# Optimization experiments

Hardware: AMD Instinct MI355X
Metric: run time of the kernel (lower is better)

The kernel has to match this reference:

```python
import jax, jax.numpy as jnp
import numpy as np

B, DIM, H, W = 2, 256, 64, 64
HEADS, DIM_HEAD = 8, 64
DIM_INNER = HEADS * DIM_HEAD  # 512


def setup_inputs() -> dict:
    key = jax.random.key(0)
    k1, k2, k3 = jax.random.split(key, 3)
    fmap = jax.random.normal(k1, (B, DIM, H, W), dtype=jnp.float32)
    # 1x1 convs == channel matmuls; store as [out_ch, in_ch]
    w_qkv = jax.random.normal(k2, (3 * DIM_INNER, DIM), dtype=jnp.float32) * (DIM ** -0.5)
    w_out = jax.random.normal(k3, (DIM, DIM_INNER), dtype=jnp.float32) * (DIM_INNER ** -0.5)
    return {"fmap": fmap, "w_qkv": w_qkv, "w_out": w_out}


def reference(fmap, w_qkv, w_out):
    b, c, x, y = fmap.shape
    n = x * y
    h, d = HEADS, DIM_HEAD
    xt = fmap.reshape(b, c, n)                       # [B, C, N]
    qkv = jnp.einsum('oc,bcn->bon', w_qkv, xt)        # [B, 3*h*d, N]
    q, k, v = jnp.split(qkv, 3, axis=1)               # each [B, h*d, N]
    # -> [B, h, N, d]
    to_bhnd = lambda t: t.reshape(b, h, d, n).transpose(0, 1, 3, 2)
    q, k, v = to_bhnd(q), to_bhnd(k), to_bhnd(v)
    # Euclidean distance matrix (torch.cdist p=2)
    q2 = jnp.sum(q * q, axis=-1)                      # [B, h, N]
    k2 = jnp.sum(k * k, axis=-1)                      # [B, h, N]
    qk = jnp.einsum('bhid,bhjd->bhij', q, k)          # [B, h, N, N]
    sim = jnp.sqrt(jnp.maximum(q2[..., :, None] + k2[..., None, :] - 2.0 * qk, 0.0))
    attn = jax.nn.softmax(sim, axis=-1)
    out = jnp.einsum('bhij,bhjd->bhid', attn, v)      # [B, h, N, d]
    out = out.transpose(0, 1, 3, 2).reshape(b, h * d, n)  # [B, h*d, N]
    out = jnp.einsum('oc,bcn->bon', w_out, out)       # [B, dim, N]
    return out.reshape(b, c, x, y)
```

## Files before the change

### kernel.cpp

```cpp
#include <hip/hip_runtime.h>

#define B_      2
#define DIM_    256
#define N_      4096
#define HEADS_  8
#define DINNER_ 512

typedef _Float16 half_t;
typedef _Float16 half8  __attribute__((ext_vector_type(8)));
typedef _Float16 half4v __attribute__((ext_vector_type(4)));
typedef _Float16 half2v __attribute__((ext_vector_type(2)));
typedef float    floatx4 __attribute__((ext_vector_type(4)));

#define SCL_    1.4426950408889634f
#define SHIFT2_ 20.0f


__global__ __launch_bounds__(256) void prep_all(const float* __restrict__ fmap,
                                                const float* __restrict__ w_qkv,
                                                const float* __restrict__ w_out,
                                                half_t* __restrict__ wqF,
                                                half_t* __restrict__ woF,
                                                half_t* __restrict__ xTg) {
    const int t = threadIdx.x, bx = blockIdx.x;
    __shared__ float Tl[64 * 68];
    if (bx < 96) {
        half_t* dst = wqF + (size_t)bx * 4096;
#pragma unroll
        for (int j = 0; j < 2; ++j) {
            const int cch = j * 256 + t;
            const int o = cch >> 4, m15 = cch & 15;
            const float4 a  = *(const float4*)&w_qkv[(size_t)(bx * 16 + m15) * 256 + o * 8];
            const float4 bb = *(const float4*)&w_qkv[(size_t)(bx * 16 + m15) * 256 + o * 8 + 4];
            half8 hv;
            hv[0] = (half_t)a.x;  hv[1] = (half_t)a.y;  hv[2] = (half_t)a.z;  hv[3] = (half_t)a.w;
            hv[4] = (half_t)bb.x; hv[5] = (half_t)bb.y; hv[6] = (half_t)bb.z; hv[7] = (half_t)bb.w;
            *(half8*)(dst + o * 128 + m15 * 8) = hv;
        }
    } else if (bx < 112) {
        const int mt = bx - 96;
        half_t* dst = woF + (size_t)mt * 8192;
#pragma unroll
        for (int j = 0; j < 4; ++j) {
            const int cch = j * 256 + t;
            const int o = cch >> 4, m15 = cch & 15;
            const float4 a  = *(const float4*)&w_out[(size_t)(mt * 16 + m15) * 512 + o * 8];
            const float4 bb = *(const float4*)&w_out[(size_t)(mt * 16 + m15) * 512 + o * 8 + 4];
            half8 hv;
            hv[0] = (half_t)a.x;  hv[1] = (half_t)a.y;  hv[2] = (half_t)a.z;  hv[3] = (half_t)a.w;
            hv[4] = (half_t)bb.x; hv[5] = (half_t)bb.y; hv[6] = (half_t)bb.z; hv[7] = (half_t)bb.w;
            *(half8*)(dst + o * 128 + m15 * 8) = hv;
        }
    } else {
        const int idx = bx - 112;
        const int n0 = (idx & 63) * 64, k0 = ((idx >> 6) & 3) * 64, b = idx >> 8;
        {
            const int kk = t >> 2, nq = (t & 3) * 16;
#pragma unroll
            for (int q = 0; q < 4; ++q) {
                float4 v = *(const float4*)&fmap[((size_t)b * DIM_ + k0 + kk) * N_ + n0 + nq + 4 * q];
                *(float4*)&Tl[kk * 68 + nq + 4 * q] = v;
            }
        }
        __syncthreads();
        {
            const int n = t >> 2, ko = (t & 3) * 16;
            half8 h0, h1;
#pragma unroll
            for (int j = 0; j < 8; ++j) h0[j] = (half_t)Tl[(ko + j) * 68 + n];
#pragma unroll
            for (int j = 0; j < 8; ++j) h1[j] = (half_t)Tl[(ko + 8 + j) * 68 + n];
            half_t* dst = xTg + (((size_t)b * 64 + (n0 >> 6)) * 4 + (k0 >> 6)) * 4096;
            const int o0 = ((ko >> 5) * 4 + (n >> 4)) * 512 + (((ko >> 3) & 3) * 16 + (n & 15)) * 8;
            const int k8 = ko + 8;
            const int o1 = ((k8 >> 5) * 4 + (n >> 4)) * 512 + (((k8 >> 3) & 3) * 16 + (n & 15)) * 8;
            *(half8*)(dst + o0) = h0;
            *(half8*)(dst + o1) = h1;
        }
    }
}

__global__ __launch_bounds__(256) void mm_qkv_mf(const half_t* __restrict__ wqF,
                                                 const half_t* __restrict__ xTg,
                                                 half_t* __restrict__ perm,
                                                 float* __restrict__ sq) {
    const int nt64 = blockIdx.x, by = blockIdx.y, b = blockIdx.z;
    const int t = threadIdx.x, w = t >> 6, L = t & 63, c = L & 15, g = L >> 4;
    const int mt = by * 4 + w;

    const half_t* Ab = wqF + (size_t)mt * 4096;
    const half_t* Bb = xTg + (((size_t)b * 64 + nt64) * 4) * 4096;

    __shared__ __align__(16) char smraw[16384];
    half_t* Bsh = (half_t*)smraw;
    half_t* VtH = (half_t*)smraw;
    float*  red = (float*)(smraw + 8192);

    const floatx4 fz = {0.f, 0.f, 0.f, 0.f};
    floatx4 acc[4];
#pragma unroll
    for (int ns = 0; ns < 4; ++ns) acc[ns] = fz;

#pragma unroll
    for (int ph = 0; ph < 2; ++ph) {
        if (ph) __syncthreads();
#pragma unroll
        for (int j = 0; j < 4; ++j)
            *(half8*)&Bsh[(j * 256 + t) * 8] = *(const half8*)(Bb + ph * 8192 + (j * 256 + t) * 8);
        __syncthreads();
#pragma unroll
        for (int kk = 0; kk < 4; ++kk) {
            const int kc = ph * 4 + kk;
            const half8 af = *(const half8*)(Ab + (kc * 4 + g) * 128 + c * 8);
            const half_t* Bs = Bsh + (kk >> 1) * 4096 + (kk & 1) * 2048;
#pragma unroll
            for (int ns = 0; ns < 4; ++ns) {
                const half8 bf = *(const half8*)(Bs + ns * 512 + L * 8);
                acc[ns] = __builtin_amdgcn_mfma_f32_16x16x32_f16(af, bf, acc[ns], 0, 0, 0);
            }
        }
    }
    __syncthreads();

    half_t* dst = perm + (((size_t)(b * 24 + by) * 64 + nt64) << 12);
    if (by < 16) {
        const float qs = (by < 8) ? -2.0f : 1.0f;
        float part[4];
#pragma unroll
        for (int ns = 0; ns < 4; ++ns) {
            half_t m[4];
            float s = 0.f;
#pragma unroll
            for (int i = 0; i < 4; ++i) {
                const half_t hq = (half_t)(acc[ns][i] * SCL_);
                const float f = (float)hq;
                s = fmaf(f, f, s);
                m[i] = (half_t)(qs * f);
            }
            part[ns] = s;
            const int off = ((w >> 1) * 4 + ns) * 512 + (((2 * w + (g >> 1)) & 3) * 16 + c) * 8 + 4 * (g & 1);
            half2v p0v, p1v;
            p0v[0] = m[0]; p0v[1] = m[1];
            p1v[0] = m[2]; p1v[1] = m[3];
            *(half2v*)(VtH + off)     = p0v;
            *(half2v*)(VtH + off + 2) = p1v;
        }
#pragma unroll
        for (int ns = 0; ns < 4; ++ns)
            red[(ns * 16 + (w * 4 + g)) * 17 + c] = part[ns];
        __syncthreads();
#pragma unroll
        for (int j = 0; j < 2; ++j)
            *(half8*)(dst + t * 16 + j * 8) = *(half8*)(VtH + t * 16 + j * 8);
        if (t < 64) {
            const int ns = t >> 4, cc = t & 15;
            float s = 0.f;
#pragma unroll
            for (int wg = 0; wg < 16; ++wg) s += red[(ns * 16 + wg) * 17 + cc];
            const int tens = by >> 3, hh = by & 7;
            sq[((size_t)(tens * 16 + b * 8 + hh)) * N_ + nt64 * 64 + ns * 16 + cc] = s;
        }
    } else {
#pragma unroll
        for (int ns = 0; ns < 4; ++ns)
#pragma unroll
            for (int i = 0; i < 4; ++i)
                VtH[((ns >> 1) * 4 + w) * 512 + ((c >> 2) * 16 + 4 * g + i) * 8 + (ns & 1) * 4 + (c & 3)] =
                    (half_t)acc[ns][i];
        __syncthreads();
#pragma unroll
        for (int j = 0; j < 2; ++j)
            *(half8*)(dst + t * 16 + j * 8) = *(half8*)(VtH + t * 16 + j * 8);
    }
}

__global__ __launch_bounds__(512) void attn_mfma(const half_t* __restrict__ perm,
                                                 const float* __restrict__ sq,
                                                 half_t* __restrict__ oh,
                                                 float* __restrict__ lbuf) {
    const int bx = blockIdx.x;
    const int qb = bx & 15, kh = bx >> 4;
    const int h = blockIdx.y, b = blockIdx.z;
    const int bh = b * HEADS_ + h;

    const half_t* Qb = perm + ((size_t)(b * 24 + h) << 18);
    const half_t* Kb = perm + ((size_t)(b * 24 + 8 + h) << 18);
    const half_t* Vb = perm + ((size_t)(b * 24 + 16 + h) << 18);
    const float* q2a = sq + (size_t)bh * N_;
    const float* k2a = sq + (size_t)(16 + bh) * N_;

    __shared__ __align__(16) half_t Kl[2][4096];
    __shared__ __align__(16) half_t Vl[2][4096];
    __shared__ __align__(16) unsigned int k2lp[1024];

    const int t = threadIdx.x, w = t >> 6, L = t & 63, c = L & 15, g = L >> 4;
    const floatx4 fz = {0.f, 0.f, 0.f, 0.f};

    {
        const float2 kv = *(const float2*)&k2a[kh * 1024 + t * 2];
        const half_t h0 = (half_t)kv.x; const half_t l0 = (half_t)(kv.x - (float)h0);
        const half_t h1 = (half_t)kv.y; const half_t l1 = (half_t)(kv.y - (float)h1);
        k2lp[t * 2]     = (unsigned)__builtin_bit_cast(unsigned short, h0) |
                          ((unsigned)__builtin_bit_cast(unsigned short, l0) << 16);
        k2lp[t * 2 + 1] = (unsigned)__builtin_bit_cast(unsigned short, h1) |
                          ((unsigned)__builtin_bit_cast(unsigned short, l1) << 16);
    }

    const int tl = w >> 1;
    const int p0 = (w & 1) * 2, p1 = p0 + 1;
    const half_t* Qt = Qb + ((size_t)(qb * 4 + tl) << 12);
    const half8 bq0a = *(const half8*)(Qt + (0 * 4 + p0) * 512 + L * 8);
    const half8 bq1a = *(const half8*)(Qt + (1 * 4 + p0) * 512 + L * 8);
    const half8 bq0b = *(const half8*)(Qt + (0 * 4 + p1) * 512 + L * 8);
    const half8 bq1b = *(const half8*)(Qt + (1 * 4 + p1) * 512 + L * 8);

    union U8 { half8 v; unsigned int u[4]; };
    U8 qXa, qXb;
    {
        const float q2la = q2a[qb * 256 + 64 * tl + 16 * p0 + c];
        const float q2lb = q2a[qb * 256 + 64 * tl + 16 * p1 + c];
        const half_t ha = (half_t)q2la; const half_t la = (half_t)(q2la - (float)ha);
        const half_t hb = (half_t)q2lb; const half_t lb_ = (half_t)(q2lb - (float)hb);
        const unsigned pka = (unsigned)__builtin_bit_cast(unsigned short, ha) |
                             ((unsigned)__builtin_bit_cast(unsigned short, la) << 16);
        const unsigned pkb = (unsigned)__builtin_bit_cast(unsigned short, hb) |
                             ((unsigned)__builtin_bit_cast(unsigned short, lb_) << 16);
        const bool lo16 = (L < 16);
        qXa.u[0] = lo16 ? pka : 0u; qXa.u[1] = lo16 ? 0x3C003C00u : 0u;
        qXa.u[2] = 0u; qXa.u[3] = 0u;
        qXb.u[0] = lo16 ? pkb : 0u; qXb.u[1] = lo16 ? 0x3C003C00u : 0u;
        qXb.u[2] = 0u; qXb.u[3] = 0u;
    }

    half8 aone8;
    {
        const half_t ov = (c == 0) ? (half_t)1.0f : (half_t)0.0f;
        aone8[0] = ov; aone8[1] = ov; aone8[2] = ov; aone8[3] = ov;
        aone8[4] = ov; aone8[5] = ov; aone8[6] = ov; aone8[7] = ov;
    }

    floatx4 Oa[4], Ob[4];
    floatx4 laca = fz, lacb = fz;
#pragma unroll
    for (int dt = 0; dt < 4; ++dt) { Oa[dt] = fz; Ob[dt] = fz; }

    const int kt0 = kh * 16;
    half8 rk = *(const half8*)(Kb + ((size_t)kt0 << 12) + t * 8);
    half8 rv = *(const half8*)(Vb + ((size_t)kt0 << 12) + t * 8);

    union H8 { half8 v; half2v h2[4]; };

#define QKC(J, SA, SB) { \
    const half8 ak0 = *(const half8*)(&Kl[buf][(0 * 4 + (J)) * 512 + L * 8]); \
    const half8 ak1 = *(const half8*)(&Kl[buf][(1 * 4 + (J)) * 512 + L * 8]); \
    U8 kX; kX.u[0] = 0x3C003C00u; kX.u[1] = k2lp[it * 64 + (J) * 16 + c]; \
    kX.u[2] = 0u; kX.u[3] = 0u; \
    SA = __builtin_amdgcn_mfma_f32_16x16x32_f16(ak0, bq0a, fz, 0, 0, 0); \
    SA = __builtin_amdgcn_mfma_f32_16x16x32_f16(ak1, bq1a, SA, 0, 0, 0); \
    SA = __builtin_amdgcn_mfma_f32_16x16x32_f16(kX.v, qXa.v, SA, 0, 0, 0); \
    SB = __builtin_amdgcn_mfma_f32_16x16x32_f16(ak0, bq0b, fz, 0, 0, 0); \
    SB = __builtin_amdgcn_mfma_f32_16x16x32_f16(ak1, bq1b, SB, 0, 0, 0); \
    SB = __builtin_amdgcn_mfma_f32_16x16x32_f16(kX.v, qXb.v, SB, 0, 0, 0); }

#define SMX(SA, SB, SLOT, UA, UB) { \
    float pa[4], pb[4]; \
    _Pragma("unroll") \
    for (int i = 0; i < 4; ++i) { \
        pa[i] = __builtin_amdgcn_exp2f(__builtin_amdgcn_sqrtf(__builtin_fabsf(SA[i])) - SHIFT2_); \
        pb[i] = __builtin_amdgcn_exp2f(__builtin_amdgcn_sqrtf(__builtin_fabsf(SB[i])) - SHIFT2_); } \
    UA.h2[2 * (SLOT)]     = __builtin_bit_cast(half2v, __builtin_amdgcn_cvt_pkrtz(pa[0], pa[1])); \
    UA.h2[2 * (SLOT) + 1] = __builtin_bit_cast(half2v, __builtin_amdgcn_cvt_pkrtz(pa[2], pa[3])); \
    UB.h2[2 * (SLOT)]     = __builtin_bit_cast(half2v, __builtin_amdgcn_cvt_pkrtz(pb[0], pb[1])); \
    UB.h2[2 * (SLOT) + 1] = __builtin_bit_cast(half2v, __builtin_amdgcn_cvt_pkrtz(pb[2], pb[3])); }

#define LPV(NTP, UA, UB) { \
    laca = __builtin_amdgcn_mfma_f32_16x16x32_f16(aone8, UA.v, laca, 0, 0, 0); \
    lacb = __builtin_amdgcn_mfma_f32_16x16x32_f16(aone8, UB.v, lacb, 0, 0, 0); \
    _Pragma("unroll") \
    for (int dt = 0; dt < 4; ++dt) { \
        const half8 av = *(const half8*)(&Vl[buf][((NTP) * 4 + dt) * 512 + L * 8]); \
        Oa[dt] = __builtin_amdgcn_mfma_f32_16x16x32_f16(av, UA.v, Oa[dt], 0, 0, 0); \
        Ob[dt] = __builtin_amdgcn_mfma_f32_16x16x32_f16(av, UB.v, Ob[dt], 0, 0, 0); } }

    for (int it = 0; it < 16; ++it) {
        const int buf = it & 1;
        *(half8*)(&Kl[buf][t * 8]) = rk;
        *(half8*)(&Vl[buf][t * 8]) = rv;
        asm volatile("s_waitcnt lgkmcnt(0)\n\ts_barrier" ::: "memory");
        if (it < 15) {
            rk = *(const half8*)(Kb + ((size_t)(kt0 + it + 1) << 12) + t * 8);
            rv = *(const half8*)(Vb + ((size_t)(kt0 + it + 1) << 12) + t * 8);
        }

        floatx4 S0a, S0b, S1a, S1b, S2a, S2b, S3a, S3b;
        H8 u0a, u0b, u1a, u1b;
        QKC(0, S0a, S0b)
        QKC(1, S1a, S1b)
        SMX(S0a, S0b, 0, u0a, u0b)
        QKC(2, S2a, S2b)
        SMX(S1a, S1b, 1, u0a, u0b)
        QKC(3, S3a, S3b)
        SMX(S2a, S2b, 0, u1a, u1b)
        LPV(0, u0a, u0b)
        SMX(S3a, S3b, 1, u1a, u1b)
        LPV(1, u1a, u1b)
    }
#undef QKC
#undef SMX
#undef LPV

    const int ntile = qb * 4 + tl;
    half_t* dst = oh + (size_t)kh * 4194304 + (((size_t)bh * 64 + ntile) << 12);
#pragma unroll
    for (int dt = 0; dt < 4; ++dt) {
        const int obase = ((dt >> 1) * 4) * 512 + (((2 * dt + (g >> 1)) & 3) * 16 + c) * 8 + 4 * (g & 1);
        const half2v a0 = __builtin_bit_cast(half2v, __builtin_amdgcn_cvt_pkrtz(Oa[dt][0], Oa[dt][1]));
        const half2v a1 = __builtin_bit_cast(half2v, __builtin_amdgcn_cvt_pkrtz(Oa[dt][2], Oa[dt][3]));
        *(half2v*)(dst + obase + p0 * 512)     = a0;
        *(half2v*)(dst + obase + p0 * 512 + 2) = a1;
        const half2v b0 = __builtin_bit_cast(half2v, __builtin_amdgcn_cvt_pkrtz(Ob[dt][0], Ob[dt][1]));
        const half2v b1 = __builtin_bit_cast(half2v, __builtin_amdgcn_cvt_pkrtz(Ob[dt][2], Ob[dt][3]));
        *(half2v*)(dst + obase + p1 * 512)     = b0;
        *(half2v*)(dst + obase + p1 * 512 + 2) = b1;
    }
    if (L < 16) {
        const size_t lb0 = (size_t)kh * 65536 + (size_t)bh * N_ + qb * 256 + 64 * tl;
        lbuf[lb0 + 16 * p0 + L] = laca[0];
        lbuf[lb0 + 16 * p1 + L] = lacb[0];
    }
}

__global__ __launch_bounds__(256) void mm_out_mf(const half_t* __restrict__ woF,
                                                 const half_t* __restrict__ oh,
                                                 const float* __restrict__ lbuf,
                                                 float* __restrict__ out) {
    const int nt64 = blockIdx.x, mb = blockIdx.y, b = blockIdx.z;
    const int t = threadIdx.x, w = t >> 6, L = t & 63, c = L & 15, g = L >> 4;
    const int mt = mb * 4 + w;

    const half_t* Ab = woF + (size_t)mt * 8192;
    const floatx4 fz = {0.f, 0.f, 0.f, 0.f};
    floatx4 O4[4];
#pragma unroll
    for (int ns = 0; ns < 4; ++ns) O4[ns] = fz;

    __shared__ __align__(16) half_t sh[2][4096];
    __shared__ float lsh[2][64];

    half8 r0[4], r1[4];
    float lr[4];

    auto LOADH = [&](int h) {
        const size_t toff = (((size_t)(b * 8 + h) * 64 + nt64) << 12) + t * 16;
#pragma unroll
        for (int q = 0; q < 4; ++q) {
            r0[q] = *(const half8*)(oh + (size_t)q * 4194304 + toff);
            r1[q] = *(const half8*)(oh + (size_t)q * 4194304 + toff + 8);
        }
        if (t < 64) {
            const size_t li = (size_t)(b * 8 + h) * N_ + nt64 * 64 + t;
#pragma unroll
            for (int q = 0; q < 4; ++q) lr[q] = lbuf[(size_t)q * 65536 + li];
        }
    };

    LOADH(0);
    for (int h = 0; h < 8; ++h) {
        const int buf = h & 1;
        const half8 s0 = (r0[0] + r0[1]) + (r0[2] + r0[3]);
        const half8 s1 = (r1[0] + r1[1]) + (r1[2] + r1[3]);
        *(half8*)(&sh[buf][t * 16])     = s0;
        *(half8*)(&sh[buf][t * 16 + 8]) = s1;
        if (t < 64)
            lsh[buf][t] = __builtin_amdgcn_rcpf((lr[0] + lr[1]) + (lr[2] + lr[3]));
        __syncthreads();
        if (h < 7) LOADH(h + 1);

        floatx4 acc[4];
#pragma unroll
        for (int ns = 0; ns < 4; ++ns) acc[ns] = fz;
#pragma unroll
        for (int c2 = 0; c2 < 2; ++c2) {
            const half8 af = *(const half8*)(Ab + (h * 8 + c2 * 4 + g) * 128 + c * 8);
#pragma unroll
            for (int ns = 0; ns < 4; ++ns) {
                const half8 bf = *(const half8*)(&sh[buf][(c2 * 4 + ns) * 512 + L * 8]);
                acc[ns] = __builtin_amdgcn_mfma_f32_16x16x32_f16(af, bf, acc[ns], 0, 0, 0);
            }
        }
#pragma unroll
        for (int ns = 0; ns < 4; ++ns) {
            const float inv = lsh[buf][ns * 16 + c];
#pragma unroll
            for (int i = 0; i < 4; ++i) O4[ns][i] = fmaf(acc[ns][i], inv, O4[ns][i]);
        }
    }

    float* Cg = out + ((size_t)b * DIM_ + mt * 16) * N_ + nt64 * 64;
#pragma unroll
    for (int ns = 0; ns < 4; ++ns)
#pragma unroll
        for (int i = 0; i < 4; ++i)
            Cg[(size_t)(4 * g + i) * N_ + ns * 16 + c] = O4[ns][i];
}

extern "C" void kernel_launch(void* const* d_in, const int* in_sizes, int n_in,
                              void* d_out, int out_size, void* d_ws, size_t ws_size,
                              hipStream_t stream) {
    const float* fmap  = (const float*)d_in[0];
    const float* w_qkv = (const float*)d_in[1];
    const float* w_out = (const float*)d_in[2];
    float* out = (float*)d_out;

    char* ws = (char*)d_ws;
    half_t* perm = (half_t*)ws;
    float*  sq   = (float*) (ws + 25165824);
    float*  lbuf = (float*) (ws + 25690112);
    half_t* woF  = (half_t*)(ws + 26738688);
    half_t* oh   = (half_t*)(ws + 27000832);
    half_t* xTg  = (half_t*)(ws + 27000832);
    half_t* wqF  = (half_t*)(ws + 31195136);

    prep_all <<<624, 256, 0, stream>>>(fmap, w_qkv, w_out, wqF, woF, xTg);
    mm_qkv_mf<<<dim3(64, 24, 2), 256, 0, stream>>>(wqF, xTg, perm, sq);
    attn_mfma<<<dim3(64, 8, 2), 512, 0, stream>>>(perm, sq, oh, lbuf);
    mm_out_mf<<<dim3(64, 4, 2), 256, 0, stream>>>(woF, oh, lbuf, out);
}
```

Before: 196.6 us.

## Double M-tile per block in QKV GEMM, split out-proj N tiles, sched attn loop

The QKV projection kernel now computes two 64-row output tiles per block, reusing each staged B tile from shared memory for twice the MFMA work. The grid is halved and the epilogue runs twice. The output projection splits each 64-column tile into two 32-column halves, doubling the block count for more parallelism, at the cost of re-reading the weights. The attention inner loop moves one PV step earlier and adds sched_group_barrier hints to interleave MFMA with VALU and LDS ops. Together these change register pressure and occupancy.

```diff
diff --git a/kernel.cpp b/kernel.cpp
--- a/kernel.cpp
+++ b/kernel.cpp
@@ -84,12 +84,12 @@
                                                  const half_t* __restrict__ xTg,
                                                  half_t* __restrict__ perm,
                                                  float* __restrict__ sq) {
-    const int nt64 = blockIdx.x, by = blockIdx.y, b = blockIdx.z;
+    const int nt64 = blockIdx.x, by2 = blockIdx.y, b = blockIdx.z;
     const int t = threadIdx.x, w = t >> 6, L = t & 63, c = L & 15, g = L >> 4;
-    const int mt = by * 4 + w;
-
-    const half_t* Ab = wqF + (size_t)mt * 4096;
-    const half_t* Bb = xTg + (((size_t)b * 64 + nt64) * 4) * 4096;
+
+    const half_t* Ab0 = wqF + (size_t)(8 * by2 + w) * 4096;
+    const half_t* Ab1 = Ab0 + 4 * 4096;
+    const half_t* Bb  = xTg + (((size_t)b * 64 + nt64) * 4) * 4096;
 
     __shared__ __align__(16) char smraw[16384];
     half_t* Bsh = (half_t*)smraw;
@@ -97,9 +97,9 @@
     float*  red = (float*)(smraw + 8192);
 
     const floatx4 fz = {0.f, 0.f, 0.f, 0.f};
-    floatx4 acc[4];
-#pragma unroll
-    for (int ns = 0; ns < 4; ++ns) acc[ns] = fz;
+    floatx4 acc0[4], acc1[4];
+#pragma unroll
+    for (int ns = 0; ns < 4; ++ns) { acc0[ns] = fz; acc1[ns] = fz; }
 
 #pragma unroll
     for (int ph = 0; ph < 2; ++ph) {
@@ -111,66 +111,76 @@
 #pragma unroll
         for (int kk = 0; kk < 4; ++kk) {
             const int kc = ph * 4 + kk;
-            const half8 af = *(const half8*)(Ab + (kc * 4 + g) * 128 + c * 8);
+            const half8 af0 = *(const half8*)(Ab0 + (kc * 4 + g) * 128 + c * 8);
+            const half8 af1 = *(const half8*)(Ab1 + (kc * 4 + g) * 128 + c * 8);
             const half_t* Bs = Bsh + (kk >> 1) * 4096 + (kk & 1) * 2048;
 #pragma unroll
             for (int ns = 0; ns < 4; ++ns) {
                 const half8 bf = *(const half8*)(Bs + ns * 512 + L * 8);
-                acc[ns] = __builtin_amdgcn_mfma_f32_16x16x32_f16(af, bf, acc[ns], 0, 0, 0);
+                acc0[ns] = __builtin_amdgcn_mfma_f32_16x16x32_f16(af0, bf, acc0[ns], 0, 0, 0);
+                acc1[ns] = __builtin_amdgcn_mfma_f32_16x16x32_f16(af1, bf, acc1[ns], 0, 0, 0);
             }
         }
     }
     __syncthreads();
 
-    half_t* dst = perm + (((size_t)(b * 24 + by) * 64 + nt64) << 12);
-    if (by < 16) {
-        const float qs = (by < 8) ? -2.0f : 1.0f;
-        float part[4];
-#pragma unroll
-        for (int ns = 0; ns < 4; ++ns) {
-            half_t m[4];
-            float s = 0.f;
-#pragma unroll
-            for (int i = 0; i < 4; ++i) {
-                const half_t hq = (half_t)(acc[ns][i] * SCL_);
-                const float f = (float)hq;
-                s = fmaf(f, f, s);
-                m[i] = (half_t)(qs * f);
-            }
-            part[ns] = s;
-            const int off = ((w >> 1) * 4 + ns) * 512 + (((2 * w + (g >> 1)) & 3) * 16 + c) * 8 + 4 * (g & 1);
-            half2v p0v, p1v;
-            p0v[0] = m[0]; p0v[1] = m[1];
-            p1v[0] = m[2]; p1v[1] = m[3];
-            *(half2v*)(VtH + off)     = p0v;
-            *(half2v*)(VtH + off + 2) = p1v;
-        }
-#pragma unroll
-        for (int ns = 0; ns < 4; ++ns)
-            red[(ns * 16 + (w * 4 + g)) * 17 + c] = part[ns];
-        __syncthreads();
-#pragma unroll
-        for (int j = 0; j < 2; ++j)
-            *(half8*)(dst + t * 16 + j * 8) = *(half8*)(VtH + t * 16 + j * 8);
-        if (t < 64) {
-            const int ns = t >> 4, cc = t & 15;
-            float s = 0.f;
-#pragma unroll
-            for (int wg = 0; wg < 16; ++wg) s += red[(ns * 16 + wg) * 17 + cc];
-            const int tens = by >> 3, hh = by & 7;
-            sq[((size_t)(tens * 16 + b * 8 + hh)) * N_ + nt64 * 64 + ns * 16 + cc] = s;
-        }
-    } else {
-#pragma unroll
-        for (int ns = 0; ns < 4; ++ns)
-#pragma unroll
-            for (int i = 0; i < 4; ++i)
-                VtH[((ns >> 1) * 4 + w) * 512 + ((c >> 2) * 16 + 4 * g + i) * 8 + (ns & 1) * 4 + (c & 3)] =
-                    (half_t)acc[ns][i];
-        __syncthreads();
-#pragma unroll
-        for (int j = 0; j < 2; ++j)
-            *(half8*)(dst + t * 16 + j * 8) = *(half8*)(VtH + t * 16 + j * 8);
+#pragma unroll
+    for (int e = 0; e < 2; ++e) {
+        if (e) __syncthreads();
+        const int by = by2 * 2 + e;
+        half_t* dst = perm + (((size_t)(b * 24 + by) * 64 + nt64) << 12);
+        if (by < 16) {
+            const float qs = (by < 8) ? -2.0f : 1.0f;
+            float part[4];
+#pragma unroll
+            for (int ns = 0; ns < 4; ++ns) {
+                const floatx4 av4 = e ? acc1[ns] : acc0[ns];
+                half_t m[4];
+                float s = 0.f;
+#pragma unroll
+                for (int i = 0; i < 4; ++i) {
+                    const half_t hq = (half_t)(av4[i] * SCL_);
+                    const float f = (float)hq;
+                    s = fmaf(f, f, s);
+                    m[i] = (half_t)(qs * f);
+                }
+                part[ns] = s;
+                const int off = ((w >> 1) * 4 + ns) * 512 + (((2 * w + (g >> 1)) & 3) * 16 + c) * 8 + 4 * (g & 1);
+                half2v p0v, p1v;
+                p0v[0] = m[0]; p0v[1] = m[1];
+                p1v[0] = m[2]; p1v[1] = m[3];
+                *(half2v*)(VtH + off)     = p0v;
+                *(half2v*)(VtH + off + 2) = p1v;
+            }
+#pragma unroll
+            for (int ns = 0; ns < 4; ++ns)
+                red[(ns * 16 + (w * 4 + g)) * 17 + c] = part[ns];
+            __syncthreads();
+#pragma unroll
+            for (int j = 0; j < 2; ++j)
+                *(half8*)(dst + t * 16 + j * 8) = *(half8*)(VtH + t * 16 + j * 8);
+            if (t < 64) {
+                const int ns = t >> 4, cc = t & 15;
+                float s = 0.f;
+#pragma unroll
+                for (int wg = 0; wg < 16; ++wg) s += red[(ns * 16 + wg) * 17 + cc];
+                const int tens = by >> 3, hh = by & 7;
+                sq[((size_t)(tens * 16 + b * 8 + hh)) * N_ + nt64 * 64 + ns * 16 + cc] = s;
+            }
+        } else {
+#pragma unroll
+            for (int ns = 0; ns < 4; ++ns) {
+                const floatx4 av4 = e ? acc1[ns] : acc0[ns];
+#pragma unroll
+                for (int i = 0; i < 4; ++i)
+                    VtH[((ns >> 1) * 4 + w) * 512 + ((c >> 2) * 16 + 4 * g + i) * 8 + (ns & 1) * 4 + (c & 3)] =
+                        (half_t)av4[i];
+            }
+            __syncthreads();
+#pragma unroll
+            for (int j = 0; j < 2; ++j)
+                *(half8*)(dst + t * 16 + j * 8) = *(half8*)(VtH + t * 16 + j * 8);
+        }
     }
 }
 
@@ -300,10 +310,18 @@
         QKC(2, S2a, S2b)
         SMX(S1a, S1b, 1, u0a, u0b)
         QKC(3, S3a, S3b)
+        LPV(0, u0a, u0b)
         SMX(S2a, S2b, 0, u1a, u1b)
-        LPV(0, u0a, u0b)
         SMX(S3a, S3b, 1, u1a, u1b)
         LPV(1, u1a, u1b)
+
+#pragma unroll
+        for (int sg = 0; sg < 44; ++sg) {
+            __builtin_amdgcn_sched_group_barrier(0x008, 1, 0);
+            __builtin_amdgcn_sched_group_barrier(0x002, 3, 0);
+            if ((sg & 3) == 1)
+                __builtin_amdgcn_sched_group_barrier(0x100, 2, 0);
+        }
     }
 #undef QKC
 #undef SMX
@@ -334,31 +352,31 @@
                                                  const half_t* __restrict__ oh,
                                                  const float* __restrict__ lbuf,
                                                  float* __restrict__ out) {
-    const int nt64 = blockIdx.x, mb = blockIdx.y, b = blockIdx.z;
+    const int bx = blockIdx.x;
+    const int nt = bx >> 1, hf = bx & 1;
+    const int mb = blockIdx.y, b = blockIdx.z;
     const int t = threadIdx.x, w = t >> 6, L = t & 63, c = L & 15, g = L >> 4;
     const int mt = mb * 4 + w;
 
     const half_t* Ab = woF + (size_t)mt * 8192;
     const floatx4 fz = {0.f, 0.f, 0.f, 0.f};
-    floatx4 O4[4];
-#pragma unroll
-    for (int ns = 0; ns < 4; ++ns) O4[ns] = fz;
-
-    __shared__ __align__(16) half_t sh[2][4096];
-    __shared__ float lsh[2][64];
-
-    half8 r0[4], r1[4];
+    floatx4 O4[2];
+    O4[0] = fz; O4[1] = fz;
+
+    __shared__ __align__(16) half_t sh[2][2048];
+    __shared__ float lsh[2][32];
+
+    half8 r0[4];
     float lr[4];
+    const int srcoff = (t >> 7) * 2048 + hf * 1024 + ((t * 8) & 1023);
 
     auto LOADH = [&](int h) {
-        const size_t toff = (((size_t)(b * 8 + h) * 64 + nt64) << 12) + t * 16;
-#pragma unroll
-        for (int q = 0; q < 4; ++q) {
-            r0[q] = *(const half8*)(oh + (size_t)q * 4194304 + toff);
-            r1[q] = *(const half8*)(oh + (size_t)q * 4194304 + toff + 8);
-        }
-        if (t < 64) {
-            const size_t li = (size_t)(b * 8 + h) * N_ + nt64 * 64 + t;
+        const size_t base = ((((size_t)(b * 8 + h) * 64 + nt) << 12)) + srcoff;
+#pragma unroll
+        for (int q = 0; q < 4; ++q)
+            r0[q] = *(const half8*)(oh + (size_t)q * 4194304 + base);
+        if (t < 32) {
+            const size_t li = (size_t)(b * 8 + h) * N_ + nt * 64 + hf * 32 + t;
 #pragma unroll
             for (int q = 0; q < 4; ++q) lr[q] = lbuf[(size_t)q * 65536 + li];
         }
@@ -368,37 +386,34 @@
     for (int h = 0; h < 8; ++h) {
         const int buf = h & 1;
         const half8 s0 = (r0[0] + r0[1]) + (r0[2] + r0[3]);
-        const half8 s1 = (r1[0] + r1[1]) + (r1[2] + r1[3]);
-        *(half8*)(&sh[buf][t * 16])     = s0;
-        *(half8*)(&sh[buf][t * 16 + 8]) = s1;
-        if (t < 64)
+        *(half8*)(&sh[buf][t * 8]) = s0;
+        if (t < 32)
             lsh[buf][t] = __builtin_amdgcn_rcpf((lr[0] + lr[1]) + (lr[2] + lr[3]));
         __syncthreads();
         if (h < 7) LOADH(h + 1);
 
-        floatx4 acc[4];
-#pragma unroll
-        for (int ns = 0; ns < 4; ++ns) acc[ns] = fz;
+        floatx4 acc[2];
+        acc[0] = fz; acc[1] = fz;
 #pragma unroll
         for (int c2 = 0; c2 < 2; ++c2) {
             const half8 af = *(const half8*)(Ab + (h * 8 + c2 * 4 + g) * 128 + c * 8);
 #pragma unroll
-            for (int ns = 0; ns < 4; ++ns) {
-                const half8 bf = *(const half8*)(&sh[buf][(c2 * 4 + ns) * 512 + L * 8]);
+            for (int ns = 0; ns < 2; ++ns) {
+                const half8 bf = *(const half8*)(&sh[buf][(c2 * 2 + ns) * 512 + L * 8]);
                 acc[ns] = __builtin_amdgcn_mfma_f32_16x16x32_f16(af, bf, acc[ns], 0, 0, 0);
             }
         }
 #pragma unroll
-        for (int ns = 0; ns < 4; ++ns) {
+        for (int ns = 0; ns < 2; ++ns) {
             const float inv = lsh[buf][ns * 16 + c];
 #pragma unroll
             for (int i = 0; i < 4; ++i) O4[ns][i] = fmaf(acc[ns][i], inv, O4[ns][i]);
         }
     }
 
-    float* Cg = out + ((size_t)b * DIM_ + mt * 16) * N_ + nt64 * 64;
-#pragma unroll
-    for (int ns = 0; ns < 4; ++ns)
+    float* Cg = out + ((size_t)b * DIM_ + mt * 16) * N_ + nt * 64 + hf * 32;
+#pragma unroll
+    for (int ns = 0; ns < 2; ++ns)
 #pragma unroll
         for (int i = 0; i < 4; ++i)
             Cg[(size_t)(4 * g + i) * N_ + ns * 16 + c] = O4[ns][i];
@@ -422,7 +437,7 @@
     half_t* wqF  = (half_t*)(ws + 31195136);
 
     prep_all <<<624, 256, 0, stream>>>(fmap, w_qkv, w_out, wqF, woF, xTg);
-    mm_qkv_mf<<<dim3(64, 24, 2), 256, 0, stream>>>(wqF, xTg, perm, sq);
+    mm_qkv_mf<<<dim3(64, 12, 2), 256, 0, stream>>>(wqF, xTg, perm, sq);
     attn_mfma<<<dim3(64, 8, 2), 512, 0, stream>>>(perm, sq, oh, lbuf);
-    mm_out_mf<<<dim3(64, 4, 2), 256, 0, stream>>>(woF, oh, lbuf, out);
+    mm_out_mf<<<dim3(128, 4, 2), 256, 0, stream>>>(woF, oh, lbuf, out);
 }
```

New measurement: 188.8 us. 1.04x faster.
